# Optimization experiments

Measured on AMD Instinct MI355X. Metric: run time of the kernel, lower is better.

Reference implementation:

```python
import jax, jax.numpy as jnp
import numpy as np

# ---- architecture constants ----
SENSOR = 128          # u feature width
B_LAYERS = 5          # branch MLP: 4 tanh hidden + 1 linear out
B_UNITS = 1024
LORA = 64
TU = 128              # trunk hidden units
TL = 4                # trunk dense layers
TRUNK_DIMS = [1] + [TU] * (TL - 1) + [1]   # 1 -> 128 -> 128 -> 128 -> 1
NO_TRUNK_PARAMS = sum(d_out + d_in * d_out for d_in, d_out in zip(TRUNK_DIMS[:-1], TRUNK_DIMS[1:]))  # 33409
T0, TFINAL = 0.0, 1.0
BATCH = 2048


def setup_inputs() -> dict:
    key = jax.random.key(0)
    ks = jax.random.split(key, 16)
    def glorot(k, shape):
        fan_in, fan_out = shape[0], shape[1]
        s = jnp.sqrt(2.0 / (fan_in + fan_out)).astype(jnp.float32)
        return jax.random.normal(k, shape, dtype=jnp.float32) * s
    inp = {
        "t": jax.random.uniform(ks[0], (BATCH, 1), dtype=jnp.float32),
        "u": jax.random.normal(ks[1], (BATCH, SENSOR), dtype=jnp.float32),
        # branch MLP: Dense(1024)+tanh x4, then Dense(1024)
        "bw0": glorot(ks[2], (SENSOR, B_UNITS)), "bb0": jnp.zeros((B_UNITS,), jnp.float32),
        "bw1": glorot(ks[3], (B_UNITS, B_UNITS)), "bb1": jnp.zeros((B_UNITS,), jnp.float32),
        "bw2": glorot(ks[4], (B_UNITS, B_UNITS)), "bb2": jnp.zeros((B_UNITS,), jnp.float32),
        "bw3": glorot(ks[5], (B_UNITS, B_UNITS)), "bb3": jnp.zeros((B_UNITS,), jnp.float32),
        "bw4": glorot(ks[6], (B_UNITS, B_UNITS)), "bb4": jnp.zeros((B_UNITS,), jnp.float32),
        # LoRA factors generating trunk params
        "W1": glorot(ks[7], (B_UNITS, LORA)),
        "W2": glorot(ks[8], (LORA, NO_TRUNK_PARAMS)),
    }
    return inp


def _slice_trunk(p):
    """Split per-sample flat trunk params [B,P] into (kernel,bias) per layer.
    Flax tree_flatten order per Dense: bias then kernel."""
    layers = []
    k = 0
    for d_in, d_out in zip(TRUNK_DIMS[:-1], TRUNK_DIMS[1:]):
        b = p[:, k:k + d_out]; k += d_out
        W = p[:, k:k + d_in * d_out].reshape(-1, d_in, d_out); k += d_in * d_out
        layers.append((W, b))
    return layers


def reference(t, u, bw0, bb0, bw1, bb1, bw2, bb2, bw3, bb3, bw4, bb4, W1, W2):
    q0 = u[:, :1]                                     # [B,1]
    # branch MLP (hypernetwork body)
    net = u
    for W, b in ((bw0, bb0), (bw1, bb1), (bw2, bb2), (bw3, bb3)):
        net = jnp.tanh(net @ W + b)
    net = net @ bw4 + bb4                             # [B, units]
    # LoRA-generated per-sample trunk params
    params = net @ (W1 @ W2)                          # [B, NO_TRUNK_PARAMS]
    # batched per-sample trunk MLP on t[i] (vectorized form of the Python loop)
    x = t                                             # [B,1]
    trunk_layers = _slice_trunk(params)
    for i, (W, b) in enumerate(trunk_layers):
        x = jnp.einsum('bi,bio->bo', x, W) + b
        if i < TL - 1:
            x = jnp.tanh(x)
    q = x                                             # [B,1]
    # hard constraint: u0 + (t-t0)/(tfinal-t0)*nn
    out = q0 + (t - T0) / (TFINAL - T0) * q           # [B,1]
    return out.reshape(-1)
```

## Files before the change

kernel.cpp:

```cpp
#include <hip/hip_runtime.h>
#include <hip/hip_bf16.h>
#include <stdint.h>

typedef unsigned short u16;
typedef unsigned int   u32;
typedef short s16x8 __attribute__((ext_vector_type(8)));
typedef float f32x4 __attribute__((ext_vector_type(4)));

#define LDP 33409

__device__ __forceinline__ u16 f2bf(float f) {
    union { float f; u32 u; } v; v.f = f;
    u32 r = v.u + 0x7fffu + ((v.u >> 16) & 1u);
    return (u16)(r >> 16);
}
__device__ __forceinline__ float bf2f(u16 h) {
    union { u32 u; float f; } v; v.u = ((u32)h) << 16;
    return v.f;
}
__device__ __forceinline__ float fast_tanh(float x) {
    float e = __expf(2.0f * x);
    return 1.0f - 2.0f / (e + 1.0f);
}
__device__ __forceinline__ f32x4 MFMA(s16x8 a, s16x8 b, f32x4 c) {
    return __builtin_amdgcn_mfma_f32_16x16x32_bf16(a, b, c, 0, 0, 0);
}
__device__ __forceinline__ void gload_lds16(const void* g, void* l) {
    __builtin_amdgcn_global_load_lds(
        (const __attribute__((address_space(1))) u32*)(uintptr_t)g,
        (__attribute__((address_space(3))) u32*)(uintptr_t)l, 16, 0, 0);
}

__global__ __launch_bounds__(256)
void prep_all(const float* __restrict__ u,
              const float* __restrict__ bw0, const float* __restrict__ bw1,
              const float* __restrict__ bw2, const float* __restrict__ bw3,
              const float* __restrict__ bw4, const float* __restrict__ bb4,
              const float* __restrict__ W1,  const float* __restrict__ W2,
              u16* __restrict__ ubf, u16* __restrict__ bw0t,
              u16* __restrict__ bw1t, u16* __restrict__ bw2t,
              u16* __restrict__ bw3t, u16* __restrict__ BWt,
              float* __restrict__ bz, u16* __restrict__ Btb)
{
    __shared__ __align__(16) char ldsbuf[33280];
    const int bid = blockIdx.x, tid = threadIdx.x;

    if (bid < 128) {
        int i = (bid * 256 + tid) * 8;
        float4 a = *(const float4*)&u[i];
        float4 b = *(const float4*)&u[i + 4];
        uint4 o;
        o.x = (u32)f2bf(a.x) | ((u32)f2bf(a.y) << 16);
        o.y = (u32)f2bf(a.z) | ((u32)f2bf(a.w) << 16);
        o.z = (u32)f2bf(b.x) | ((u32)f2bf(b.y) << 16);
        o.w = (u32)f2bf(b.z) | ((u32)f2bf(b.w) << 16);
        *(uint4*)&ubf[i] = o;
    } else if (bid < 928) {
        float (*tile)[65] = (float(*)[65])ldsbuf;
        const float* src; u16* dst; int ldsrc, lddst, rb, cb;
        if (bid < 160) {
            int idx = bid - 128;
            src = bw0; dst = bw0t; ldsrc = 1024; lddst = 128;
            rb = (idx >> 4) * 64; cb = (idx & 15) * 64;
        } else {
            int idx = bid - 160;
            int layer = idx >> 8, w = idx & 255;
            src = layer == 0 ? bw1 : (layer == 1 ? bw2 : bw3);
            dst = layer == 0 ? bw1t : (layer == 1 ? bw2t : bw3t);
            ldsrc = 1024; lddst = 1024;
            rb = (w >> 4) * 64; cb = (w & 15) * 64;
        }
        for (int i = tid; i < 64 * 64; i += 256) {
            int r = i >> 6, c = i & 63;
            tile[r][c] = src[(size_t)(rb + r) * ldsrc + cb + c];
        }
        __syncthreads();
        for (int i = tid; i < 64 * 64; i += 256) {
            int c = i >> 6, r = i & 63;
            dst[(size_t)(cb + c) * lddst + rb + r] = f2bf(tile[r][c]);
        }
    } else if (bid < 1185) {
        int lb = bid - 928;
        if (lb == 256) {
            if (tid < 64) {
                float a = 0.f;
                for (int j = 0; j < 1024; ++j) a = fmaf(bb4[j], W1[j * 64 + tid], a);
                bz[tid] = a;
            }
            return;
        }
        const int n = tid & 63;
        const int k = lb * 4 + (tid >> 6);
        float a = 0.f;
        for (int j = 0; j < 1024; ++j) a = fmaf(bw4[(size_t)k * 1024 + j], W1[j * 64 + n], a);
        BWt[(size_t)n * 1024 + k] = f2bf(a);
    } else {
        float (*tile)[130] = (float(*)[130])ldsbuf;
        int idx = bid - 1185;
        int layer = idx / 129, pbi = idx % 129;
        u16* Bt = Btb + (size_t)layer * 128 * 8256;
        const int colbase = layer ? 16896 : 384, biasbase = layer ? 16768 : 256;
        const int pb = pbi * 64;
        for (int i = tid; i < 64 * 128; i += 256) {
            int p = pb + (i >> 7), n = i & 127;
            float v = (p < 8192)
                ? W2[(size_t)(p & 63) * LDP + colbase + (size_t)(p >> 6) * 128 + n]
                : W2[(size_t)(p - 8192) * LDP + biasbase + n];
            tile[i >> 7][n] = v;
        }
        __syncthreads();
        for (int i = tid; i < 64 * 128; i += 256) {
            int n = i >> 6, dp = i & 63;
            Bt[(size_t)n * 8256 + pb + dp] = f2bf(tile[dp][n]);
        }
    }
}

__global__ __launch_bounds__(256, 2)
void gemm_branch(const u16* __restrict__ A, int lda,
                 const u16* __restrict__ Bt, int ldb,
                 const float* __restrict__ bias,
                 u16* __restrict__ Cout, int ldc, int K)
{
    __shared__ __align__(16) u16 As[2][64 * 32];
    __shared__ __align__(16) u16 Bs[2][64 * 32];
    const int tid = threadIdx.x, lane = tid & 63, wid = tid >> 6;
    const int wr = wid >> 1, wc = wid & 1;
    const int bn = blockIdx.x * 64, bm = blockIdx.y * 64;
    const int NT = K >> 5;
    const int arow = tid >> 2, ck = tid & 3;
    const u16* aSrc = A + (size_t)(bm + arow) * lda + (ck ^ (arow & 3)) * 8;
    const u16* bSrc = Bt + (size_t)(bn + arow) * ldb + (ck ^ (arow & 3)) * 8;
    f32x4 acc[2][2] = {};

    auto STAGE = [&](int buf, int t) {
        const int k0 = t << 5;
        gload_lds16(aSrc + k0, (char*)As[buf] + wid * 1024);
        gload_lds16(bSrc + k0, (char*)Bs[buf] + wid * 1024);
    };
    auto COMPUTE = [&](int buf) {
        s16x8 a[2], b[2];
        #pragma unroll
        for (int mi = 0; mi < 2; ++mi) {
            int row = wr * 32 + mi * 16 + (lane & 15);
            int s = (lane >> 4) ^ (row & 3);
            a[mi] = *(const s16x8*)&As[buf][row * 32 + s * 8];
        }
        #pragma unroll
        for (int ni = 0; ni < 2; ++ni) {
            int n = wc * 32 + ni * 16 + (lane & 15);
            int s = (lane >> 4) ^ (n & 3);
            b[ni] = *(const s16x8*)&Bs[buf][n * 32 + s * 8];
        }
        #pragma unroll
        for (int mi = 0; mi < 2; ++mi)
        #pragma unroll
        for (int ni = 0; ni < 2; ++ni)
            acc[mi][ni] = MFMA(a[mi], b[ni], acc[mi][ni]);
    };

    STAGE(0, 0);
    __syncthreads();
    for (int t = 0; t < NT; ++t) {
        if (t + 1 < NT) STAGE((t + 1) & 1, t + 1);
        COMPUTE(t & 1);
        __syncthreads();
    }

    #pragma unroll
    for (int mi = 0; mi < 2; ++mi)
    #pragma unroll
    for (int ni = 0; ni < 2; ++ni) {
        const int col = bn + wc * 32 + ni * 16 + (lane & 15);
        const float bv = bias[col];
        #pragma unroll
        for (int jj = 0; jj < 4; ++jj) {
            const int row = bm + wr * 32 + mi * 16 + (lane >> 4) * 4 + jj;
            Cout[(size_t)row * ldc + col] = f2bf(fast_tanh(acc[mi][ni][jj] + bv));
        }
    }
}

__global__ __launch_bounds__(256, 2)
void zgemm(const u16* __restrict__ A, const u16* __restrict__ Bt,
           float* __restrict__ zc)
{
    __shared__ __align__(16) u16 As[2][64 * 32];
    __shared__ __align__(16) u16 Bs[2][64 * 32];
    const int tid = threadIdx.x, lane = tid & 63, wid = tid >> 6;
    const int wr = wid >> 1, wc = wid & 1;
    const int bm = blockIdx.y * 64, kz = blockIdx.z;
    const int t0 = kz * 4, nt = 4;
    const int arow = tid >> 2, ck = tid & 3;
    const u16* aSrc = A + (size_t)(bm + arow) * 1024 + (ck ^ (arow & 3)) * 8;
    const u16* bSrc = Bt + (size_t)arow * 1024 + (ck ^ (arow & 3)) * 8;
    f32x4 acc[2][2] = {};

    auto STAGE = [&](int buf, int t) {
        const int k0 = t << 5;
        gload_lds16(aSrc + k0, (char*)As[buf] + wid * 1024);
        gload_lds16(bSrc + k0, (char*)Bs[buf] + wid * 1024);
    };
    auto COMPUTE = [&](int buf) {
        s16x8 a[2];
        #pragma unroll
        for (int mi = 0; mi < 2; ++mi) {
            int row = wr * 32 + mi * 16 + (lane & 15);
            int s = (lane >> 4) ^ (row & 3);
            a[mi] = *(const s16x8*)&As[buf][row * 32 + s * 8];
        }
        #pragma unroll
        for (int ni = 0; ni < 2; ++ni) {
            int n = wc * 32 + ni * 16 + (lane & 15);
            int s = (lane >> 4) ^ (n & 3);
            s16x8 b = *(const s16x8*)&Bs[buf][n * 32 + s * 8];
            #pragma unroll
            for (int mi = 0; mi < 2; ++mi)
                acc[mi][ni] = MFMA(a[mi], b, acc[mi][ni]);
        }
    };

    STAGE(0, t0);
    __syncthreads();
    for (int t = 0; t < nt; ++t) {
        if (t + 1 < nt) STAGE((t + 1) & 1, t0 + t + 1);
        COMPUTE(t & 1);
        __syncthreads();
    }
    #pragma unroll
    for (int mi = 0; mi < 2; ++mi)
    #pragma unroll
    for (int ni = 0; ni < 2; ++ni) {
        const int col = wc * 32 + ni * 16 + (lane & 15);
        #pragma unroll
        for (int jj = 0; jj < 4; ++jj) {
            const int row = bm + wr * 32 + mi * 16 + (lane >> 4) * 4 + jj;
            zc[((size_t)kz * 2048 + row) * 64 + col] = acc[mi][ni][jj];
        }
    }
}

__global__ __launch_bounds__(256)
void z_l1_h1(const float* __restrict__ zc, const float* __restrict__ bz,
             const float* __restrict__ W2, const float* __restrict__ t,
             u16* __restrict__ z, u16* __restrict__ h1)
{
    __shared__ float zsh[32][64];
    const int rb = blockIdx.x * 32;
    #pragma unroll
    for (int ii = 0; ii < 8; ++ii) {
        int e = ii * 256 + threadIdx.x;
        int r = e >> 6, k = e & 63;
        size_t off = (size_t)(rb + r) * 64 + k;
        float s = bz[k];
        #pragma unroll
        for (int sk = 0; sk < 8; ++sk) s += zc[(size_t)sk * 2048 * 64 + off];
        zsh[r][k] = s;
        z[off] = f2bf(s);
    }
    __syncthreads();
    const int o = threadIdx.x & 127;
    const int rh = (threadIdx.x >> 7) * 16;
    float acc_a[16] = {}, acc_b[16] = {};
    for (int k = 0; k < 64; ++k) {
        float wa = W2[(size_t)k * LDP + o];
        float wb = W2[(size_t)k * LDP + 128 + o];
        #pragma unroll
        for (int r = 0; r < 16; ++r) {
            float zv = zsh[rh + r][k];
            acc_a[r] = fmaf(zv, wa, acc_a[r]);
            acc_b[r] = fmaf(zv, wb, acc_b[r]);
        }
    }
    #pragma unroll
    for (int r = 0; r < 16; ++r) {
        int b = rb + rh + r;
        h1[b * 128 + o] = f2bf(fast_tanh(t[b] * acc_b[r] + acc_a[r]));
    }
}

__global__ __launch_bounds__(512, 2)
void trunk128(const u16* __restrict__ h, const u16* __restrict__ z,
              const u16* __restrict__ Bt, float* __restrict__ Cp)
{
    constexpr int NT = 258, SKT = 16;
    __shared__ __align__(16) u16 As[2][128 * 32];
    __shared__ __align__(16) u16 Bs[2][128 * 32];
    const int tid = threadIdx.x, lane = tid & 63, wid = tid >> 6;
    const int wr = wid >> 1, wc = wid & 1;
    const int bm = blockIdx.x * 128, kz = blockIdx.y;
    const int t0 = (NT * kz) / SKT, t1 = (NT * (kz + 1)) / SKT;
    const int arow = tid >> 2, ck = tid & 3;
    const int b = bm + arow;
    const s16x8 zlo = *(const s16x8*)&z[b * 64 + ck * 8];
    const s16x8 zhi = *(const s16x8*)&z[b * 64 + 32 + ck * 8];
    const int slot = (ck ^ (arow & 3)) * 8;
    f32x4 acc[2][4] = {};

    auto STAGE = [&](int buf, int t) {
        const int p0 = t << 5;
        gload_lds16(Bt + (size_t)arow * 8256 + p0 + (ck ^ (arow & 3)) * 8,
                    (char*)Bs[buf] + wid * 1024);
        const s16x8 zv = (p0 & 32) ? zhi : zlo;
        u16 o8[8];
        if (p0 < 8192) {
            const float hf = bf2f(h[b * 128 + (p0 >> 6)]);
            #pragma unroll
            for (int j = 0; j < 8; ++j) o8[j] = f2bf(hf * bf2f((u16)zv[j]));
        } else {
            #pragma unroll
            for (int j = 0; j < 8; ++j) o8[j] = (u16)zv[j];
        }
        *(s16x8*)&As[buf][arow * 32 + slot] = *(s16x8*)o8;
    };
    auto COMPUTE = [&](int buf) {
        s16x8 a[2], bb[4];
        #pragma unroll
        for (int mi = 0; mi < 2; ++mi) {
            int row = wr * 32 + mi * 16 + (lane & 15);
            int s = (lane >> 4) ^ (row & 3);
            a[mi] = *(const s16x8*)&As[buf][row * 32 + s * 8];
        }
        #pragma unroll
        for (int ni = 0; ni < 4; ++ni) {
            int n = wc * 64 + ni * 16 + (lane & 15);
            int s = (lane >> 4) ^ (n & 3);
            bb[ni] = *(const s16x8*)&Bs[buf][n * 32 + s * 8];
        }
        #pragma unroll
        for (int mi = 0; mi < 2; ++mi)
        #pragma unroll
        for (int ni = 0; ni < 4; ++ni)
            acc[mi][ni] = MFMA(a[mi], bb[ni], acc[mi][ni]);
    };

    STAGE(0, t0);
    __syncthreads();
    const int nt = t1 - t0;
    for (int t = 0; t < nt; ++t) {
        if (t + 1 < nt) STAGE((t + 1) & 1, t0 + t + 1);
        COMPUTE(t & 1);
        __syncthreads();
    }

    #pragma unroll
    for (int mi = 0; mi < 2; ++mi)
    #pragma unroll
    for (int ni = 0; ni < 4; ++ni) {
        const int col = wc * 64 + ni * 16 + (lane & 15);
        #pragma unroll
        for (int jj = 0; jj < 4; ++jj) {
            const int row = bm + wr * 32 + mi * 16 + (lane >> 4) * 4 + jj;
            Cp[((size_t)kz * 2048 + row) * 128 + col] = acc[mi][ni][jj];
        }
    }
}

__global__ __launch_bounds__(256)
void reduce_tanh(const float* __restrict__ Cp, u16* __restrict__ hout) {
    const int idx = blockIdx.x * 256 + threadIdx.x;
    const size_t S = (size_t)2048 * 128;
    float s = 0.f;
    #pragma unroll
    for (int k = 0; k < 16; ++k) s += Cp[idx + k * S];
    hout[idx] = f2bf(fast_tanh(s));
}

__global__ __launch_bounds__(256)
void reduce_out(const float* __restrict__ Cp, const u16* __restrict__ z,
                const float* __restrict__ W2, const float* __restrict__ t,
                const float* __restrict__ u, float* __restrict__ out)
{
    __shared__ float sh[4][128];
    const int wv = threadIdx.x >> 6, l = threadIdx.x & 63;
    const int b = blockIdx.x * 4 + wv;
    const size_t S = (size_t)2048 * 128;
    #pragma unroll
    for (int e = l; e < 128; e += 64) {
        float s = 0.f;
        #pragma unroll
        for (int k = 0; k < 16; ++k) s += Cp[k * S + (size_t)b * 128 + e];
        sh[wv][e] = fast_tanh(s);
    }
    __syncthreads();
    const float* wrow = &W2[(size_t)l * LDP + 33280];
    float acc = wrow[0];
    #pragma unroll 8
    for (int i = 0; i < 128; ++i) acc = fmaf(sh[wv][i], wrow[1 + i], acc);
    float p = bf2f(z[b * 64 + l]) * acc;
    #pragma unroll
    for (int off = 32; off > 0; off >>= 1) p += __shfl_down(p, off);
    if (l == 0) out[b] = u[b * 128] + t[b] * p;
}

extern "C" void kernel_launch(void* const* d_in, const int* in_sizes, int n_in,
                              void* d_out, int out_size, void* d_ws, size_t ws_size,
                              hipStream_t stream)
{
    const float* t   = (const float*)d_in[0];
    const float* u   = (const float*)d_in[1];
    const float* bw0 = (const float*)d_in[2];
    const float* bb0 = (const float*)d_in[3];
    const float* bw1 = (const float*)d_in[4];
    const float* bb1 = (const float*)d_in[5];
    const float* bw2 = (const float*)d_in[6];
    const float* bb2 = (const float*)d_in[7];
    const float* bw3 = (const float*)d_in[8];
    const float* bb3 = (const float*)d_in[9];
    const float* bw4 = (const float*)d_in[10];
    const float* bb4 = (const float*)d_in[11];
    const float* W1  = (const float*)d_in[12];
    const float* W2  = (const float*)d_in[13];
    float* out = (float*)d_out;

    char* base = (char*)d_ws;
    u16*   bw1t = (u16*)(base);
    u16*   bw2t = (u16*)(base + 2097152);
    u16*   bw3t = (u16*)(base + 4194304);
    u16*   actA = (u16*)(base + 6291456);
    u16*   actB = (u16*)(base + 10485760);
    u16*   ubf  = (u16*)(base + 14680064);
    u16*   bw0t = (u16*)(base + 15204352);
    u16*   BWt  = (u16*)(base + 15499264);
    float* bz   = (float*)(base + 15630336);
    u16*   z    = (u16*)(base + 16777216);
    u16*   h1   = (u16*)(base + 17039360);
    u16*   h2   = (u16*)(base + 17563648);
    u16*   Bt   = (u16*)(base + 18087936);
    float* zc = (float*)(base);
    float* Cp = (float*)(base);

    dim3 blk(256);
    prep_all<<<1443, blk, 0, stream>>>(u, bw0, bw1, bw2, bw3, bw4, bb4, W1, W2,
                                       ubf, bw0t, bw1t, bw2t, bw3t, BWt, bz, Bt);

    gemm_branch<<<dim3(16, 32), blk, 0, stream>>>(ubf,  128,  bw0t, 128,  bb0, actA, 1024, 128);
    gemm_branch<<<dim3(16, 32), blk, 0, stream>>>(actA, 1024, bw1t, 1024, bb1, actB, 1024, 1024);
    gemm_branch<<<dim3(16, 32), blk, 0, stream>>>(actB, 1024, bw2t, 1024, bb2, actA, 1024, 1024);
    gemm_branch<<<dim3(16, 32), blk, 0, stream>>>(actA, 1024, bw3t, 1024, bb3, actB, 1024, 1024);
    zgemm<<<dim3(1, 32, 8), blk, 0, stream>>>(actB, BWt, zc);
    z_l1_h1<<<64, blk, 0, stream>>>(zc, bz, W2, t, z, h1);
    trunk128<<<dim3(16, 16), dim3(512), 0, stream>>>(h1, z, Bt, Cp);
    reduce_tanh<<<1024, blk, 0, stream>>>(Cp, h2);
    trunk128<<<dim3(16, 16), dim3(512), 0, stream>>>(h2, z, Bt + (size_t)128 * 8256, Cp);
    reduce_out<<<512, blk, 0, stream>>>(Cp, z, W2, t, u, out);
}
```

Baseline: 159.1 us.

## Overlap weight preprocessing with branch GEMMs by fusing prep work into GEMM launches

The monolithic prep kernel is split up. Each later layer's weight transpose, the bw4·W1 product and the W2 trunk-weight repacking now run as extra blocks inside the branch GEMM launches, so they overlap with the matmul work instead of running first. The bw4·W1 reduction is split across four warps with an LDS reduction, and the W2 repack uses smaller 32-row tiles. z_l1_h1 uses 16-row blocks to launch more blocks. The cost is a larger, branchier fused kernel whose extra blocks compete with the GEMM blocks for CUs and LDS.

```diff
diff --git a/kernel.cpp b/kernel.cpp
--- a/kernel.cpp
+++ b/kernel.cpp
@@ -32,19 +32,11 @@
 }
 
 __global__ __launch_bounds__(256)
-void prep_all(const float* __restrict__ u,
-              const float* __restrict__ bw0, const float* __restrict__ bw1,
-              const float* __restrict__ bw2, const float* __restrict__ bw3,
-              const float* __restrict__ bw4, const float* __restrict__ bb4,
-              const float* __restrict__ W1,  const float* __restrict__ W2,
-              u16* __restrict__ ubf, u16* __restrict__ bw0t,
-              u16* __restrict__ bw1t, u16* __restrict__ bw2t,
-              u16* __restrict__ bw3t, u16* __restrict__ BWt,
-              float* __restrict__ bz, u16* __restrict__ Btb)
-{
-    __shared__ __align__(16) char ldsbuf[33280];
+void prep0(const float* __restrict__ u, const float* __restrict__ bw0,
+           u16* __restrict__ ubf, u16* __restrict__ bw0t)
+{
+    __shared__ float tile[64][65];
     const int bid = blockIdx.x, tid = threadIdx.x;
-
     if (bid < 128) {
         int i = (bid * 256 + tid) * 8;
         float4 a = *(const float4*)&u[i];
@@ -55,53 +47,142 @@
         o.z = (u32)f2bf(b.x) | ((u32)f2bf(b.y) << 16);
         o.w = (u32)f2bf(b.z) | ((u32)f2bf(b.w) << 16);
         *(uint4*)&ubf[i] = o;
-    } else if (bid < 928) {
-        float (*tile)[65] = (float(*)[65])ldsbuf;
-        const float* src; u16* dst; int ldsrc, lddst, rb, cb;
-        if (bid < 160) {
-            int idx = bid - 128;
-            src = bw0; dst = bw0t; ldsrc = 1024; lddst = 128;
-            rb = (idx >> 4) * 64; cb = (idx & 15) * 64;
-        } else {
-            int idx = bid - 160;
-            int layer = idx >> 8, w = idx & 255;
-            src = layer == 0 ? bw1 : (layer == 1 ? bw2 : bw3);
-            dst = layer == 0 ? bw1t : (layer == 1 ? bw2t : bw3t);
-            ldsrc = 1024; lddst = 1024;
-            rb = (w >> 4) * 64; cb = (w & 15) * 64;
-        }
+        return;
+    }
+    const int idx = bid - 128;
+    const int rb = (idx >> 4) * 64, cb = (idx & 15) * 64;
+    for (int i = tid; i < 64 * 64; i += 256) {
+        int r = i >> 6, c = i & 63;
+        tile[r][c] = bw0[(size_t)(rb + r) * 1024 + cb + c];
+    }
+    __syncthreads();
+    for (int i = tid; i < 64 * 64; i += 256) {
+        int c = i >> 6, r = i & 63;
+        bw0t[(size_t)(cb + c) * 128 + rb + r] = f2bf(tile[r][c]);
+    }
+}
+
+__global__ __launch_bounds__(256, 2)
+void gemm_fused(const u16* __restrict__ A, int lda,
+                const u16* __restrict__ Bt, int ldb,
+                const float* __restrict__ bias,
+                u16* __restrict__ Cout, int ldc, int K, int mode,
+                const float* __restrict__ xsrc, u16* __restrict__ xdst,
+                const float* __restrict__ bw4, const float* __restrict__ bb4,
+                const float* __restrict__ W1, u16* __restrict__ BWt,
+                float* __restrict__ bz,
+                const float* __restrict__ W2, u16* __restrict__ Btb)
+{
+    __shared__ __align__(16) char lds[16640];
+    const int bid = blockIdx.x, tid = threadIdx.x;
+
+    if (bid < 512) {
+        u16 (*As)[64 * 32] = (u16(*)[64 * 32])lds;
+        u16 (*Bs)[64 * 32] = (u16(*)[64 * 32])(lds + 8192);
+        const int lane = tid & 63, wid = tid >> 6;
+        const int wr = wid >> 1, wc = wid & 1;
+        const int bn = (bid & 15) * 64, bm = (bid >> 4) * 64;
+        const int NT = K >> 5;
+        const int arow = tid >> 2, ck = tid & 3;
+        const u16* aSrc = A + (size_t)(bm + arow) * lda + (ck ^ (arow & 3)) * 8;
+        const u16* bSrc = Bt + (size_t)(bn + arow) * ldb + (ck ^ (arow & 3)) * 8;
+        f32x4 acc[2][2] = {};
+
+        auto STAGE = [&](int buf, int t) {
+            const int k0 = t << 5;
+            gload_lds16(aSrc + k0, (char*)As[buf] + wid * 1024);
+            gload_lds16(bSrc + k0, (char*)Bs[buf] + wid * 1024);
+        };
+        auto COMPUTE = [&](int buf) {
+            s16x8 a[2], b[2];
+            #pragma unroll
+            for (int mi = 0; mi < 2; ++mi) {
+                int row = wr * 32 + mi * 16 + (lane & 15);
+                int s = (lane >> 4) ^ (row & 3);
+                a[mi] = *(const s16x8*)&As[buf][row * 32 + s * 8];
+            }
+            #pragma unroll
+            for (int ni = 0; ni < 2; ++ni) {
+                int n = wc * 32 + ni * 16 + (lane & 15);
+                int s = (lane >> 4) ^ (n & 3);
+                b[ni] = *(const s16x8*)&Bs[buf][n * 32 + s * 8];
+            }
+            #pragma unroll
+            for (int mi = 0; mi < 2; ++mi)
+            #pragma unroll
+            for (int ni = 0; ni < 2; ++ni)
+                acc[mi][ni] = MFMA(a[mi], b[ni], acc[mi][ni]);
+        };
+
+        STAGE(0, 0);
+        __syncthreads();
+        for (int t = 0; t < NT; ++t) {
+            if (t + 1 < NT) STAGE((t + 1) & 1, t + 1);
+            COMPUTE(t & 1);
+            __syncthreads();
+        }
+        #pragma unroll
+        for (int mi = 0; mi < 2; ++mi)
+        #pragma unroll
+        for (int ni = 0; ni < 2; ++ni) {
+            const int col = bn + wc * 32 + ni * 16 + (lane & 15);
+            const float bv = bias[col];
+            #pragma unroll
+            for (int jj = 0; jj < 4; ++jj) {
+                const int row = bm + wr * 32 + mi * 16 + (lane >> 4) * 4 + jj;
+                Cout[(size_t)row * ldc + col] = f2bf(fast_tanh(acc[mi][ni][jj] + bv));
+            }
+        }
+    } else if (mode <= 2 && bid < 768) {
+        float (*tile)[65] = (float(*)[65])lds;
+        const int idx = bid - 512;
+        const int rb = (idx >> 4) * 64, cb = (idx & 15) * 64;
         for (int i = tid; i < 64 * 64; i += 256) {
             int r = i >> 6, c = i & 63;
-            tile[r][c] = src[(size_t)(rb + r) * ldsrc + cb + c];
+            tile[r][c] = xsrc[(size_t)(rb + r) * 1024 + cb + c];
         }
         __syncthreads();
         for (int i = tid; i < 64 * 64; i += 256) {
             int c = i >> 6, r = i & 63;
-            dst[(size_t)(cb + c) * lddst + rb + r] = f2bf(tile[r][c]);
-        }
-    } else if (bid < 1185) {
-        int lb = bid - 928;
-        if (lb == 256) {
-            if (tid < 64) {
-                float a = 0.f;
-                for (int j = 0; j < 1024; ++j) a = fmaf(bb4[j], W1[j * 64 + tid], a);
-                bz[tid] = a;
-            }
+            xdst[(size_t)(cb + c) * 1024 + rb + r] = f2bf(tile[r][c]);
+        }
+    } else if (mode == 2) {
+        const int lb = bid - 768;
+        const int n = tid & 63, jc = tid >> 6;
+        if (lb == 512) {
+            float (*sh1)[64] = (float(*)[64])lds;
+            float a = 0.f;
+            for (int j = jc * 256; j < jc * 256 + 256; ++j)
+                a = fmaf(bb4[j], W1[j * 64 + n], a);
+            sh1[jc][n] = a;
+            __syncthreads();
+            if (tid < 64)
+                bz[tid] = sh1[0][tid] + sh1[1][tid] + sh1[2][tid] + sh1[3][tid];
             return;
         }
-        const int n = tid & 63;
-        const int k = lb * 4 + (tid >> 6);
-        float a = 0.f;
-        for (int j = 0; j < 1024; ++j) a = fmaf(bw4[(size_t)k * 1024 + j], W1[j * 64 + n], a);
-        BWt[(size_t)n * 1024 + k] = f2bf(a);
+        float (*sh)[2][64] = (float(*)[2][64])lds;
+        const int k0 = lb * 2;
+        float a0 = 0.f, a1 = 0.f;
+        for (int j = jc * 256; j < jc * 256 + 256; ++j) {
+            float w = W1[j * 64 + n];
+            a0 = fmaf(bw4[(size_t)k0 * 1024 + j], w, a0);
+            a1 = fmaf(bw4[(size_t)(k0 + 1) * 1024 + j], w, a1);
+        }
+        sh[jc][0][n] = a0; sh[jc][1][n] = a1;
+        __syncthreads();
+        if (tid < 128) {
+            int kk = tid >> 6, nn = tid & 63;
+            float s = sh[0][kk][nn] + sh[1][kk][nn] + sh[2][kk][nn] + sh[3][kk][nn];
+            BWt[(size_t)nn * 1024 + k0 + kk] = f2bf(s);
+        }
     } else {
-        float (*tile)[130] = (float(*)[130])ldsbuf;
-        int idx = bid - 1185;
-        int layer = idx / 129, pbi = idx % 129;
-        u16* Bt = Btb + (size_t)layer * 128 * 8256;
+        float (*tile)[130] = (float(*)[130])lds;
+        const int idx = bid - 512;
+        const int layer = idx / 258, pbi = idx % 258;
+        u16* Btd = Btb + (size_t)layer * 128 * 8256;
         const int colbase = layer ? 16896 : 384, biasbase = layer ? 16768 : 256;
-        const int pb = pbi * 64;
-        for (int i = tid; i < 64 * 128; i += 256) {
+        const int pb = pbi * 32;
+        for (int i = tid; i < 32 * 128; i += 256) {
             int p = pb + (i >> 7), n = i & 127;
             float v = (p < 8192)
                 ? W2[(size_t)(p & 63) * LDP + colbase + (size_t)(p >> 6) * 128 + n]
@@ -109,74 +190,9 @@
             tile[i >> 7][n] = v;
         }
         __syncthreads();
-        for (int i = tid; i < 64 * 128; i += 256) {
-            int n = i >> 6, dp = i & 63;
-            Bt[(size_t)n * 8256 + pb + dp] = f2bf(tile[dp][n]);
-        }
-    }
-}
-
-__global__ __launch_bounds__(256, 2)
-void gemm_branch(const u16* __restrict__ A, int lda,
-                 const u16* __restrict__ Bt, int ldb,
-                 const float* __restrict__ bias,
-                 u16* __restrict__ Cout, int ldc, int K)
-{
-    __shared__ __align__(16) u16 As[2][64 * 32];
-    __shared__ __align__(16) u16 Bs[2][64 * 32];
-    const int tid = threadIdx.x, lane = tid & 63, wid = tid >> 6;
-    const int wr = wid >> 1, wc = wid & 1;
-    const int bn = blockIdx.x * 64, bm = blockIdx.y * 64;
-    const int NT = K >> 5;
-    const int arow = tid >> 2, ck = tid & 3;
-    const u16* aSrc = A + (size_t)(bm + arow) * lda + (ck ^ (arow & 3)) * 8;
-    const u16* bSrc = Bt + (size_t)(bn + arow) * ldb + (ck ^ (arow & 3)) * 8;
-    f32x4 acc[2][2] = {};
-
-    auto STAGE = [&](int buf, int t) {
-        const int k0 = t << 5;
-        gload_lds16(aSrc + k0, (char*)As[buf] + wid * 1024);
-        gload_lds16(bSrc + k0, (char*)Bs[buf] + wid * 1024);
-    };
-    auto COMPUTE = [&](int buf) {
-        s16x8 a[2], b[2];
-        #pragma unroll
-        for (int mi = 0; mi < 2; ++mi) {
-            int row = wr * 32 + mi * 16 + (lane & 15);
-            int s = (lane >> 4) ^ (row & 3);
-            a[mi] = *(const s16x8*)&As[buf][row * 32 + s * 8];
-        }
-        #pragma unroll
-        for (int ni = 0; ni < 2; ++ni) {
-            int n = wc * 32 + ni * 16 + (lane & 15);
-            int s = (lane >> 4) ^ (n & 3);
-            b[ni] = *(const s16x8*)&Bs[buf][n * 32 + s * 8];
-        }
-        #pragma unroll
-        for (int mi = 0; mi < 2; ++mi)
-        #pragma unroll
-        for (int ni = 0; ni < 2; ++ni)
-            acc[mi][ni] = MFMA(a[mi], b[ni], acc[mi][ni]);
-    };
-
-    STAGE(0, 0);
-    __syncthreads();
-    for (int t = 0; t < NT; ++t) {
-        if (t + 1 < NT) STAGE((t + 1) & 1, t + 1);
-        COMPUTE(t & 1);
-        __syncthreads();
-    }
-
-    #pragma unroll
-    for (int mi = 0; mi < 2; ++mi)
-    #pragma unroll
-    for (int ni = 0; ni < 2; ++ni) {
-        const int col = bn + wc * 32 + ni * 16 + (lane & 15);
-        const float bv = bias[col];
-        #pragma unroll
-        for (int jj = 0; jj < 4; ++jj) {
-            const int row = bm + wr * 32 + mi * 16 + (lane >> 4) * 4 + jj;
-            Cout[(size_t)row * ldc + col] = f2bf(fast_tanh(acc[mi][ni][jj] + bv));
+        for (int i = tid; i < 32 * 128; i += 256) {
+            int n = i >> 5, dp = i & 31;
+            Btd[(size_t)n * 8256 + pb + dp] = f2bf(tile[dp][n]);
         }
     }
 }
@@ -245,10 +261,10 @@
              const float* __restrict__ W2, const float* __restrict__ t,
              u16* __restrict__ z, u16* __restrict__ h1)
 {
-    __shared__ float zsh[32][64];
-    const int rb = blockIdx.x * 32;
-    #pragma unroll
-    for (int ii = 0; ii < 8; ++ii) {
+    __shared__ float zsh[16][64];
+    const int rb = blockIdx.x * 16;
+    #pragma unroll
+    for (int ii = 0; ii < 4; ++ii) {
         int e = ii * 256 + threadIdx.x;
         int r = e >> 6, k = e & 63;
         size_t off = (size_t)(rb + r) * 64 + k;
@@ -260,20 +276,20 @@
     }
     __syncthreads();
     const int o = threadIdx.x & 127;
-    const int rh = (threadIdx.x >> 7) * 16;
-    float acc_a[16] = {}, acc_b[16] = {};
+    const int rh = (threadIdx.x >> 7) * 8;
+    float acc_a[8] = {}, acc_b[8] = {};
     for (int k = 0; k < 64; ++k) {
         float wa = W2[(size_t)k * LDP + o];
         float wb = W2[(size_t)k * LDP + 128 + o];
         #pragma unroll
-        for (int r = 0; r < 16; ++r) {
+        for (int r = 0; r < 8; ++r) {
             float zv = zsh[rh + r][k];
             acc_a[r] = fmaf(zv, wa, acc_a[r]);
             acc_b[r] = fmaf(zv, wb, acc_b[r]);
         }
     }
     #pragma unroll
-    for (int r = 0; r < 16; ++r) {
+    for (int r = 0; r < 8; ++r) {
         int b = rb + rh + r;
         h1[b * 128 + o] = f2bf(fast_tanh(t[b] * acc_b[r] + acc_a[r]));
     }
@@ -431,15 +447,22 @@
     float* Cp = (float*)(base);
 
     dim3 blk(256);
-    prep_all<<<1443, blk, 0, stream>>>(u, bw0, bw1, bw2, bw3, bw4, bb4, W1, W2,
-                                       ubf, bw0t, bw1t, bw2t, bw3t, BWt, bz, Bt);
-
-    gemm_branch<<<dim3(16, 32), blk, 0, stream>>>(ubf,  128,  bw0t, 128,  bb0, actA, 1024, 128);
-    gemm_branch<<<dim3(16, 32), blk, 0, stream>>>(actA, 1024, bw1t, 1024, bb1, actB, 1024, 1024);
-    gemm_branch<<<dim3(16, 32), blk, 0, stream>>>(actB, 1024, bw2t, 1024, bb2, actA, 1024, 1024);
-    gemm_branch<<<dim3(16, 32), blk, 0, stream>>>(actA, 1024, bw3t, 1024, bb3, actB, 1024, 1024);
+    prep0<<<160, blk, 0, stream>>>(u, bw0, ubf, bw0t);
+
+    gemm_fused<<<768, blk, 0, stream>>>(
+        ubf, 128, bw0t, 128, bb0, actA, 1024, 128, 0,
+        bw1, bw1t, bw4, bb4, W1, BWt, bz, W2, Bt);
+    gemm_fused<<<768, blk, 0, stream>>>(
+        actA, 1024, bw1t, 1024, bb1, actB, 1024, 1024, 1,
+        bw2, bw2t, bw4, bb4, W1, BWt, bz, W2, Bt);
+    gemm_fused<<<1281, blk, 0, stream>>>(
+        actB, 1024, bw2t, 1024, bb2, actA, 1024, 1024, 2,
+        bw3, bw3t, bw4, bb4, W1, BWt, bz, W2, Bt);
+    gemm_fused<<<1028, blk, 0, stream>>>(
+        actA, 1024, bw3t, 1024, bb3, actB, 1024, 1024, 3,
+        nullptr, nullptr, bw4, bb4, W1, BWt, bz, W2, Bt);
     zgemm<<<dim3(1, 32, 8), blk, 0, stream>>>(actB, BWt, zc);
-    z_l1_h1<<<64, blk, 0, stream>>>(zc, bz, W2, t, z, h1);
+    z_l1_h1<<<128, blk, 0, stream>>>(zc, bz, W2, t, z, h1);
     trunk128<<<dim3(16, 16), dim3(512), 0, stream>>>(h1, z, Bt, Cp);
     reduce_tanh<<<1024, blk, 0, stream>>>(Cp, h2);
     trunk128<<<dim3(16, 16), dim3(512), 0, stream>>>(h2, z, Bt + (size_t)128 * 8256, Cp);
```

Result: faster. 138.5 us (-13.0%).
